# Kernel optimization log

Measured on AMD Instinct MI355X. Metric: run time of the kernel, lower is better.

## Reference

```python
import jax, jax.numpy as jnp
import numpy as np

N_NODES = 10000
N_EDGES = 640000
N_GRAPHS = 64
IN_FEAT = 128
HID = (128, 128)
NUM_CLASS = 10


def setup_inputs() -> dict:
    key = jax.random.key(0)
    ks = jax.random.split(key, 10)
    x = jax.random.normal(ks[0], (N_NODES, IN_FEAT), dtype=jnp.float32)
    edge_index = jax.random.randint(ks[1], (2, N_EDGES), 0, N_NODES, dtype=jnp.int64)
    batch = jnp.sort(jax.random.randint(ks[2], (N_NODES,), 0, N_GRAPHS, dtype=jnp.int64))
    # GCNConv weights (PyG applies x @ W then propagates, bias added after aggregation)
    s1 = 1.0 / np.sqrt(IN_FEAT)
    s2 = 1.0 / np.sqrt(HID[0])
    s3 = 1.0 / np.sqrt(HID[1])
    W1 = jax.random.uniform(ks[3], (IN_FEAT, HID[0]), jnp.float32, -s1, s1)
    b1 = jnp.zeros((HID[0],), jnp.float32)
    W2 = jax.random.uniform(ks[4], (HID[0], HID[1]), jnp.float32, -s2, s2)
    b2 = jnp.zeros((HID[1],), jnp.float32)
    Wlin = jax.random.uniform(ks[5], (HID[1], NUM_CLASS), jnp.float32, -s3, s3)
    blin = jax.random.uniform(ks[6], (NUM_CLASS,), jnp.float32, -s3, s3)
    return {"x": x, "edge_index": edge_index, "batch": batch,
            "W1": W1, "b1": b1, "W2": W2, "b2": b2, "Wlin": Wlin, "blin": blin}


def _gcn_conv(x, src, dst, W, b):
    # GCNConv with self-loops and symmetric normalization:
    # out[i] = sum_{(j->i) in E} d[j]^{-1/2} d[i]^{-1/2} (x_j W) + d[i]^{-1} (x_i W) + b
    # where d = in-degree (on dst) + 1 for the self-loop.
    h = x @ W                                                      # [N, F]
    ones = jnp.ones(src.shape[0], dtype=h.dtype)
    deg = jax.ops.segment_sum(ones, dst, num_segments=x.shape[0]) + 1.0
    dinv = jax.lax.rsqrt(deg)                                      # [N]
    norm = dinv[src] * dinv[dst]                                   # [E]
    agg = jax.ops.segment_sum(h[src] * norm[:, None], dst, num_segments=x.shape[0])
    agg = agg + h * (dinv * dinv)[:, None]                         # self-loop term
    return agg + b


def _global_mean_pool(x, batch, num_graphs):
    sums = jax.ops.segment_sum(x, batch, num_segments=num_graphs)          # [G, F]
    cnt = jax.ops.segment_sum(jnp.ones(x.shape[0], x.dtype), batch, num_segments=num_graphs)
    return sums / jnp.maximum(cnt, 1.0)[:, None]


def reference(x, edge_index, batch, W1, b1, W2, b2, Wlin, blin):
    src, dst = edge_index[0], edge_index[1]
    h = jax.nn.relu(_gcn_conv(x, src, dst, W1, b1))
    h = jax.nn.relu(_gcn_conv(h, src, dst, W2, b2))
    g = _global_mean_pool(h, batch, N_GRAPHS)      # [G, hid1]
    return g @ Wlin + blin                          # [G, num_class]
```

## Files before the change

kernel.cpp:

```cpp
#include <hip/hip_runtime.h>

#define NN 10000
#define NE 640000
#define NG 64
#define NF 128
#define NC 10
#define TMR 16
#define TKC 32
#define NB 250
#define BSZ 40
#define G1 512
#define ECHUNK 1250
#define CAP 32
#define CCAP 3072
#define NSL 64
#define MAXD 192


__device__ __forceinline__ unsigned short f2bf(float f) {
    unsigned int u = __float_as_uint(f);
    return (unsigned short)((u + 0x7FFF + ((u >> 16) & 1)) >> 16);
}
__device__ __forceinline__ float bf_lo(unsigned int p) {
    return __uint_as_float(p << 16);
}
__device__ __forceinline__ float bf_hi(unsigned int p) {
    return __uint_as_float(p & 0xFFFF0000u);
}

__device__ __forceinline__ int detect64(const int* w, long span) {
    int lane = threadIdx.x & 63;
    long e = (long)lane * (span - 1) / 63;
    return (__ballot(w[2 * e + 1] != 0) == 0ULL) ? 1 : 0;
}

__device__ __forceinline__ int ld_idx(const void* p, long i, int is64) {
    return is64 ? (int)((const long long*)p)[i] : ((const int*)p)[i];
}

__global__ __launch_bounds__(256) void k_prep(const void* __restrict__ ei,
                                              const void* __restrict__ batch,
                                              int* __restrict__ bh,
                                              int* __restrict__ ebuf,
                                              float* __restrict__ outacc,
                                              float* __restrict__ cntinv) {
    int is64 = detect64((const int*)ei, NE);
    __shared__ int hist[256];
    __shared__ int cur[256];
    int tid = threadIdx.x;
    hist[tid] = 0;
    __syncthreads();
    if (blockIdx.x < 8) {
        float* base = outacc + (size_t)blockIdx.x * 8 * NG * NC;
        for (int i = tid; i < 8 * NG * NC; i += 256) base[i] = 0.f;
    }
    if (blockIdx.x == 8 && tid < NG) {
        int isb = detect64((const int*)batch, NN / 2);
        int lo0 = 0, hi0 = NN;
        while (lo0 < hi0) {
            int m = (lo0 + hi0) >> 1;
            if (ld_idx(batch, m, isb) < tid) lo0 = m + 1; else hi0 = m;
        }
        int lo1 = lo0, hi1 = NN;
        while (lo1 < hi1) {
            int m = (lo1 + hi1) >> 1;
            if (ld_idx(batch, m, isb) < tid + 1) lo1 = m + 1; else hi1 = m;
        }
        cntinv[tid] = 1.0f / fmaxf((float)(lo1 - lo0), 1.0f);
    }
    int e0 = blockIdx.x * ECHUNK;
    int dstv[5], srcv[5];
#pragma unroll
    for (int i = 0; i < 5; ++i) {
        int r = tid + i * 256;
        if (r < ECHUNK) {
            long e = (long)e0 + r;
            dstv[i] = ld_idx(ei, (long)NE + e, is64);
            srcv[i] = ld_idx(ei, e, is64);
            atomicAdd(&hist[dstv[i] / BSZ], 1);
        } else {
            dstv[i] = -1; srcv[i] = 0;
        }
    }
    __syncthreads();
    if (tid < NB) {
        bh[tid * G1 + blockIdx.x] = min(hist[tid], CAP);
        cur[tid] = (tid * G1 + blockIdx.x) * CAP;
    }
    __syncthreads();
#pragma unroll
    for (int i = 0; i < 5; ++i) {
        if (tid + i * 256 < ECHUNK) {
            int dst = dstv[i], src = srcv[i];
            int b = dst / BSZ;
            int p = atomicAdd(&cur[b], 1);
            int lim = (b * G1 + blockIdx.x) * CAP + CAP;
            if (p < lim) ebuf[p] = ((dst - b * BSZ) << 14) | src;
        }
    }
}

__global__ __launch_bounds__(256) void k_csr(const int* __restrict__ ebuf,
                                             const int* __restrict__ bh,
                                             int* __restrict__ coff,
                                             int* __restrict__ deg,
                                             float* __restrict__ dinv,
                                             unsigned short* __restrict__ csrc) {
    __shared__ int scnt[G1];
    __shared__ int cbase[G1];
    __shared__ int wsum[4];
    __shared__ int eb[CCAP];
    __shared__ int dcount[BSZ];
    __shared__ int cur[BSZ];
    int b = blockIdx.x, tid = threadIdx.x;
    int lane = tid & 63, wv = tid >> 6;
    for (int i = tid; i < G1; i += 256) scnt[i] = bh[b * G1 + i];
    if (tid < BSZ) dcount[tid] = 0;
    __syncthreads();
    int v0 = scnt[2 * tid], v1 = scnt[2 * tid + 1];
    int lsum = v0 + v1;
    int pref = lsum;
    for (int o = 1; o < 64; o <<= 1) {
        int t = __shfl_up(pref, o, 64);
        if (lane >= o) pref += t;
    }
    if (lane == 63) wsum[wv] = pref;
    __syncthreads();
    int off = 0;
#pragma unroll
    for (int j = 0; j < 4; ++j) if (j < wv) off += wsum[j];
    int ex = pref - lsum + off;
    cbase[2 * tid] = ex;
    cbase[2 * tid + 1] = ex + v0;
    int tot = wsum[0] + wsum[1] + wsum[2] + wsum[3];
    if (tot > CCAP) tot = CCAP;
    __syncthreads();
#pragma unroll
    for (int cp = 0; cp < 2; ++cp) {
        int cell = 2 * tid + cp;
        int c = scnt[cell], lb = cbase[cell];
        int gb = (b * G1 + cell) * CAP;
        if (lb + c > CCAP) c = max(0, CCAP - lb);
        for (int i = 0; i < c; ++i) eb[lb + i] = ebuf[gb + i];
    }
    __syncthreads();
    for (int i = tid; i < tot; i += 256)
        atomicAdd(&dcount[eb[i] >> 14], 1);
    __syncthreads();
    if (tid < 64) {
        int d = (tid < BSZ) ? dcount[tid] : 0;
        int pr = d;
        for (int o = 1; o < 64; o <<= 1) {
            int t = __shfl_up(pr, o, 64);
            if (tid >= o) pr += t;
        }
        if (tid < BSZ) {
            int st = pr - d;
            cur[tid] = b * CCAP + st;
            coff[b * BSZ + tid] = b * CCAP + st;
            deg[b * BSZ + tid] = d;
            dinv[b * BSZ + tid] = rsqrtf((float)d + 1.0f);
        }
    }
    __syncthreads();
    for (int i = tid; i < tot; i += 256) {
        int pk = eb[i];
        int p = atomicAdd(&cur[pk >> 14], 1);
        csrc[p] = (unsigned short)(pk & 16383);
    }
}

__global__ __launch_bounds__(256) void k_gemm(const float* __restrict__ X,
                                              const float* __restrict__ W,
                                              const float* __restrict__ dinv,
                                              unsigned short* __restrict__ Y,
                                              int nrows) {
    __shared__ float sX[TKC * 20];
    __shared__ float sW[32 * 132];
    int tid = threadIdx.x;
    int rg = tid & 7;
    int cg = tid >> 3;
    int m0 = blockIdx.x * TMR;
    float acc[2][4] = {{0.f}};
    for (int kc = 0; kc < NF / TKC; ++kc) {
        int k0 = kc * TKC;
        if (tid < 128) {
            int row = tid >> 3, kq = tid & 7;
            int mm = m0 + row; if (mm > nrows - 1) mm = nrows - 1;
            float4 v = *(const float4*)(X + (size_t)mm * NF + k0 + kq * 4);
            sX[(kq * 4 + 0) * 20 + row] = v.x;
            sX[(kq * 4 + 1) * 20 + row] = v.y;
            sX[(kq * 4 + 2) * 20 + row] = v.z;
            sX[(kq * 4 + 3) * 20 + row] = v.w;
        }
#pragma unroll
        for (int j = 0; j < 4; ++j) {
            int idx = tid + 256 * j;
            int k = idx >> 5, cq = idx & 31;
            float4 v = *(const float4*)(W + (size_t)(k0 + k) * NF + cq * 4);
            *(float4*)(sW + cq * 132 + k * 4) = v;
        }
        __syncthreads();
#pragma unroll 8
        for (int k = 0; k < TKC; ++k) {
            float2 xf = *(const float2*)(sX + k * 20 + rg * 2);
            float4 wf = *(const float4*)(sW + cg * 132 + k * 4);
            acc[0][0] = fmaf(xf.x, wf.x, acc[0][0]);
            acc[0][1] = fmaf(xf.x, wf.y, acc[0][1]);
            acc[0][2] = fmaf(xf.x, wf.z, acc[0][2]);
            acc[0][3] = fmaf(xf.x, wf.w, acc[0][3]);
            acc[1][0] = fmaf(xf.y, wf.x, acc[1][0]);
            acc[1][1] = fmaf(xf.y, wf.y, acc[1][1]);
            acc[1][2] = fmaf(xf.y, wf.z, acc[1][2]);
            acc[1][3] = fmaf(xf.y, wf.w, acc[1][3]);
        }
        __syncthreads();
    }
#pragma unroll
    for (int r = 0; r < 2; ++r) {
        int m = m0 + rg * 2 + r;
        if (m < nrows) {
            float ds = dinv[m];
            ushort4 h;
            h.x = f2bf(acc[r][0] * ds);
            h.y = f2bf(acc[r][1] * ds);
            h.z = f2bf(acc[r][2] * ds);
            h.w = f2bf(acc[r][3] * ds);
            *(ushort4*)(Y + (size_t)m * NF + cg * 4) = h;
        }
    }
}

__device__ __forceinline__ void gacc_node(const unsigned short* __restrict__ G,
                                          const unsigned short* __restrict__ csrc,
                                          unsigned short* ls,
                                          int beg, int end, int q, int f, int lane,
                                          float a[8]) {
    int dg = end - beg;
    int nst = min(dg, MAXD);
    for (int i = lane; i < nst; i += 64) ls[i] = csrc[beg + i];
    int vi = q;
    int nfull = nst & ~31;
    for (; vi < nfull; vi += 32) {
        int s[8];
#pragma unroll
        for (int j = 0; j < 8; ++j) s[j] = ls[vi + 4 * j];
        uint4 p[8];
#pragma unroll
        for (int j = 0; j < 8; ++j)
            p[j] = ((const uint4*)(G + (size_t)s[j] * NF))[f];
#pragma unroll
        for (int j = 0; j < 8; ++j) {
            a[0] += bf_lo(p[j].x); a[1] += bf_hi(p[j].x);
            a[2] += bf_lo(p[j].y); a[3] += bf_hi(p[j].y);
            a[4] += bf_lo(p[j].z); a[5] += bf_hi(p[j].z);
            a[6] += bf_lo(p[j].w); a[7] += bf_hi(p[j].w);
        }
    }
    int nfull16 = nst & ~15;
    for (; vi < nfull16; vi += 16) {
        int s[4];
#pragma unroll
        for (int j = 0; j < 4; ++j) s[j] = ls[vi + 4 * j];
        uint4 p[4];
#pragma unroll
        for (int j = 0; j < 4; ++j)
            p[j] = ((const uint4*)(G + (size_t)s[j] * NF))[f];
#pragma unroll
        for (int j = 0; j < 4; ++j) {
            a[0] += bf_lo(p[j].x); a[1] += bf_hi(p[j].x);
            a[2] += bf_lo(p[j].y); a[3] += bf_hi(p[j].y);
            a[4] += bf_lo(p[j].z); a[5] += bf_hi(p[j].z);
            a[6] += bf_lo(p[j].w); a[7] += bf_hi(p[j].w);
        }
    }
    int npad = (nst + 3) & ~3;
    for (; vi < npad; vi += 4) {
        int s = ls[min(vi, nst - 1)];
        uint4 p = ((const uint4*)(G + (size_t)s * NF))[f];
        if (vi < nst) {
            a[0] += bf_lo(p.x); a[1] += bf_hi(p.x);
            a[2] += bf_lo(p.y); a[3] += bf_hi(p.y);
            a[4] += bf_lo(p.z); a[5] += bf_hi(p.z);
            a[6] += bf_lo(p.w); a[7] += bf_hi(p.w);
        }
    }
    for (int e2 = beg + MAXD + q; e2 < end; e2 += 4) {
        int s = csrc[e2];
        uint4 p = ((const uint4*)(G + (size_t)s * NF))[f];
        a[0] += bf_lo(p.x); a[1] += bf_hi(p.x);
        a[2] += bf_lo(p.y); a[3] += bf_hi(p.y);
        a[4] += bf_lo(p.z); a[5] += bf_hi(p.z);
        a[6] += bf_lo(p.w); a[7] += bf_hi(p.w);
    }
#pragma unroll
    for (int j = 0; j < 8; ++j) a[j] += __shfl_xor(a[j], 16);
#pragma unroll
    for (int j = 0; j < 8; ++j) a[j] += __shfl_xor(a[j], 32);
}

__global__ __launch_bounds__(256, 4) void k_gather(const unsigned short* __restrict__ G,
                                                   const int* __restrict__ off,
                                                   const int* __restrict__ dg,
                                                   const unsigned short* __restrict__ csrc,
                                                   const float* __restrict__ dinv,
                                                   const float* __restrict__ bias,
                                                   float* __restrict__ OUT) {
    __shared__ unsigned short lsbuf[4][MAXD];
    int wid = threadIdx.x >> 6, lane = threadIdx.x & 63;
    int q = lane >> 4, f = lane & 15;
    int n = blockIdx.x * 4 + wid;
    if (n >= NN) return;
    int beg = off[n], end = beg + dg[n];
    float din = dinv[n];
    float a[8] = {0.f, 0.f, 0.f, 0.f, 0.f, 0.f, 0.f, 0.f};
    gacc_node(G, csrc, lsbuf[wid], beg, end, q, f, lane, a);
    if (q == 0) {
        uint4 sp = ((const uint4*)(G + (size_t)n * NF))[f];
        float4 b0 = ((const float4*)bias)[2 * f];
        float4 b1 = ((const float4*)bias)[2 * f + 1];
        float4 o0, o1;
        o0.x = fmaxf(fmaf(din, a[0] + bf_lo(sp.x), b0.x), 0.f);
        o0.y = fmaxf(fmaf(din, a[1] + bf_hi(sp.x), b0.y), 0.f);
        o0.z = fmaxf(fmaf(din, a[2] + bf_lo(sp.y), b0.z), 0.f);
        o0.w = fmaxf(fmaf(din, a[3] + bf_hi(sp.y), b0.w), 0.f);
        o1.x = fmaxf(fmaf(din, a[4] + bf_lo(sp.z), b1.x), 0.f);
        o1.y = fmaxf(fmaf(din, a[5] + bf_hi(sp.z), b1.y), 0.f);
        o1.z = fmaxf(fmaf(din, a[6] + bf_lo(sp.w), b1.z), 0.f);
        o1.w = fmaxf(fmaf(din, a[7] + bf_hi(sp.w), b1.w), 0.f);
        ((float4*)(OUT + (size_t)n * NF))[2 * f] = o0;
        ((float4*)(OUT + (size_t)n * NF))[2 * f + 1] = o1;
    }
}

__global__ __launch_bounds__(256, 4) void k_gatherpool(const unsigned short* __restrict__ G,
                                                       const int* __restrict__ off,
                                                       const int* __restrict__ dg,
                                                       const unsigned short* __restrict__ csrc,
                                                       const float* __restrict__ dinv,
                                                       const float* __restrict__ bias,
                                                       const void* __restrict__ batch,
                                                       const float* __restrict__ Wl,
                                                       const float* __restrict__ cntinv,
                                                       float* __restrict__ outacc) {
    __shared__ float sWl2[8 * NC * 16];
    __shared__ unsigned short lsbuf[4][MAXD];
    int tid = threadIdx.x;
    for (int i = tid; i < 8 * NC * 16; i += 256) {
        int j = i / (NC * 16);
        int r = i - j * (NC * 16);
        int c = r >> 4, f0 = r & 15;
        sWl2[i] = Wl[(f0 * 8 + j) * NC + c];
    }
    int isb64 = detect64((const int*)batch, NN / 2);
    int wid = tid >> 6, lane = tid & 63;
    int q = lane >> 4, f = lane & 15;
    int n = blockIdx.x * 4 + wid;
    int beg = off[n], end = beg + dg[n];
    float din = dinv[n];
    float a[8] = {0.f, 0.f, 0.f, 0.f, 0.f, 0.f, 0.f, 0.f};
    __syncthreads();
    gacc_node(G, csrc, lsbuf[wid], beg, end, q, f, lane, a);
    int g = ld_idx(batch, n, isb64);
    uint4 sp = ((const uint4*)(G + (size_t)n * NF))[f];
    float4 b0 = ((const float4*)bias)[2 * f];
    float4 b1 = ((const float4*)bias)[2 * f + 1];
    float h[8];
    h[0] = fmaxf(fmaf(din, a[0] + bf_lo(sp.x), b0.x), 0.f);
    h[1] = fmaxf(fmaf(din, a[1] + bf_hi(sp.x), b0.y), 0.f);
    h[2] = fmaxf(fmaf(din, a[2] + bf_lo(sp.y), b0.z), 0.f);
    h[3] = fmaxf(fmaf(din, a[3] + bf_hi(sp.y), b0.w), 0.f);
    h[4] = fmaxf(fmaf(din, a[4] + bf_lo(sp.z), b1.x), 0.f);
    h[5] = fmaxf(fmaf(din, a[5] + bf_hi(sp.z), b1.y), 0.f);
    h[6] = fmaxf(fmaf(din, a[6] + bf_lo(sp.w), b1.z), 0.f);
    h[7] = fmaxf(fmaf(din, a[7] + bf_hi(sp.w), b1.w), 0.f);
    float p[NC];
#pragma unroll
    for (int c = 0; c < NC; ++c) p[c] = 0.f;
#pragma unroll
    for (int j = 0; j < 8; ++j) {
        const float* wrow = sWl2 + j * (NC * 16) + f;
#pragma unroll
        for (int c = 0; c < NC; ++c) p[c] = fmaf(h[j], wrow[c * 16], p[c]);
    }
#pragma unroll
    for (int c = 0; c < NC; ++c) {
        p[c] += __shfl_xor(p[c], 1);
        p[c] += __shfl_xor(p[c], 2);
        p[c] += __shfl_xor(p[c], 4);
        p[c] += __shfl_xor(p[c], 8);
    }
    if (lane == 0) {
        float ci = cntinv[g];
        float* dst = outacc + (size_t)(blockIdx.x & (NSL - 1)) * NG * NC + g * NC;
#pragma unroll
        for (int c = 0; c < NC; ++c) atomicAdd(dst + c, p[c] * ci);
    }
}

__global__ __launch_bounds__(256) void k_fin(const float* __restrict__ outacc,
                                             const float* __restrict__ bl,
                                             float* __restrict__ out) {
    int tid = threadIdx.x;
    for (int i = tid; i < NG * NC; i += 256) {
        float s = 0.f;
#pragma unroll 8
        for (int sl = 0; sl < NSL; ++sl) s += outacc[(size_t)sl * NG * NC + i];
        out[i] = s + bl[i % NC];
    }
}

extern "C" void kernel_launch(void* const* d_in, const int* in_sizes, int n_in,
                              void* d_out, int out_size, void* d_ws, size_t ws_size,
                              hipStream_t stream) {
    const float* x  = (const float*)d_in[0];
    const void*  ei = d_in[1];
    const void*  bt = d_in[2];
    const float* W1 = (const float*)d_in[3];
    const float* b1 = (const float*)d_in[4];
    const float* W2 = (const float*)d_in[5];
    const float* b2 = (const float*)d_in[6];
    const float* Wl = (const float*)d_in[7];
    const float* bl = (const float*)d_in[8];

    char* ws = (char*)d_ws;
    int*            coff   = (int*)(ws + 0);
    int*            deg    = (int*)(ws + 40000);
    float*          dinv   = (float*)(ws + 80000);
    float*          outacc = (float*)(ws + 120000);
    float*          cntinv = (float*)(ws + 283840);
    unsigned short* csrc   = (unsigned short*)(ws + 284160);
    unsigned short* Gb     = (unsigned short*)(ws + 2201088);
    float*          bufB   = (float*)(ws + 4761088);
    int*            bh     = (int*)(ws + 2201088);
    int*            ebuf   = (int*)(ws + 4761088);

    k_prep<<<G1, 256, 0, stream>>>(ei, bt, bh, ebuf, outacc, cntinv);
    k_csr <<<NB, 256, 0, stream>>>(ebuf, bh, coff, deg, dinv, csrc);

    k_gemm<<<(NN + TMR - 1) / TMR, 256, 0, stream>>>(x, W1, dinv, Gb, NN);
    k_gather<<<(NN + 3) / 4, 256, 0, stream>>>(Gb, coff, deg, csrc, dinv, b1, bufB);
    k_gemm<<<(NN + TMR - 1) / TMR, 256, 0, stream>>>(bufB, W2, dinv, Gb, NN);
    k_gatherpool<<<(NN + 3) / 4, 256, 0, stream>>>(Gb, coff, deg, csrc, dinv, b2,
                                                   bt, Wl, cntinv, outacc);
    k_fin<<<1, 256, 0, stream>>>(outacc, bl, (float*)d_out);
}
```

Before: 165.9 us.

## Fuse first-layer GEMM into prep kernel and move source scaling into gather

The first-layer X@W1 GEMM now runs as extra blocks of the edge-preprocessing kernel, so it no longer waits for the degree computation. The source-side dinv scaling is therefore applied per edge in the first gather, using dinv values staged in shared memory alongside the neighbour indices. This drops one kernel launch and its serialization, at the cost of an extra per-edge dinv lookup and FMA in the first gather. Workspace offsets are rearranged so the GEMM output no longer overlaps buffers the prep kernel is still writing.

```diff
diff --git a/kernel.cpp b/kernel.cpp
--- a/kernel.cpp
+++ b/kernel.cpp
@@ -10,6 +10,7 @@
 #define NB 250
 #define BSZ 40
 #define G1 512
+#define GEMMB ((NN + TMR - 1) / TMR)
 #define ECHUNK 1250
 #define CAP 32
 #define CCAP 3072
@@ -38,21 +39,80 @@
     return is64 ? (int)((const long long*)p)[i] : ((const int*)p)[i];
 }
 
-__global__ __launch_bounds__(256) void k_prep(const void* __restrict__ ei,
-                                              const void* __restrict__ batch,
-                                              int* __restrict__ bh,
-                                              int* __restrict__ ebuf,
-                                              float* __restrict__ outacc,
-                                              float* __restrict__ cntinv) {
-    int is64 = detect64((const int*)ei, NE);
+__global__ __launch_bounds__(256) void k_prepgemm(const void* __restrict__ ei,
+                                                  const void* __restrict__ batch,
+                                                  int* __restrict__ bh,
+                                                  int* __restrict__ ebuf,
+                                                  float* __restrict__ outacc,
+                                                  float* __restrict__ cntinv,
+                                                  const float* __restrict__ X,
+                                                  const float* __restrict__ W,
+                                                  unsigned short* __restrict__ Y) {
     __shared__ int hist[256];
     __shared__ int cur[256];
+    __shared__ float sX[TKC * 20];
+    __shared__ float sW[32 * 132];
     int tid = threadIdx.x;
+
+    if (blockIdx.x >= G1) {
+        int m0 = (int)(blockIdx.x - G1) * TMR;
+        int rg = tid & 7;
+        int cg = tid >> 3;
+        float acc[2][4] = {{0.f}};
+        for (int kc = 0; kc < NF / TKC; ++kc) {
+            int k0 = kc * TKC;
+            if (tid < 128) {
+                int row = tid >> 3, kq = tid & 7;
+                int mm = m0 + row; if (mm > NN - 1) mm = NN - 1;
+                float4 v = *(const float4*)(X + (size_t)mm * NF + k0 + kq * 4);
+                sX[(kq * 4 + 0) * 20 + row] = v.x;
+                sX[(kq * 4 + 1) * 20 + row] = v.y;
+                sX[(kq * 4 + 2) * 20 + row] = v.z;
+                sX[(kq * 4 + 3) * 20 + row] = v.w;
+            }
+#pragma unroll
+            for (int j = 0; j < 4; ++j) {
+                int idx = tid + 256 * j;
+                int k = idx >> 5, cq = idx & 31;
+                float4 v = *(const float4*)(W + (size_t)(k0 + k) * NF + cq * 4);
+                *(float4*)(sW + cq * 132 + k * 4) = v;
+            }
+            __syncthreads();
+#pragma unroll 8
+            for (int k = 0; k < TKC; ++k) {
+                float2 xf = *(const float2*)(sX + k * 20 + rg * 2);
+                float4 wf = *(const float4*)(sW + cg * 132 + k * 4);
+                acc[0][0] = fmaf(xf.x, wf.x, acc[0][0]);
+                acc[0][1] = fmaf(xf.x, wf.y, acc[0][1]);
+                acc[0][2] = fmaf(xf.x, wf.z, acc[0][2]);
+                acc[0][3] = fmaf(xf.x, wf.w, acc[0][3]);
+                acc[1][0] = fmaf(xf.y, wf.x, acc[1][0]);
+                acc[1][1] = fmaf(xf.y, wf.y, acc[1][1]);
+                acc[1][2] = fmaf(xf.y, wf.z, acc[1][2]);
+                acc[1][3] = fmaf(xf.y, wf.w, acc[1][3]);
+            }
+            __syncthreads();
+        }
+#pragma unroll
+        for (int r = 0; r < 2; ++r) {
+            int m = m0 + rg * 2 + r;
+            if (m < NN) {
+                ushort4 h;
+                h.x = f2bf(acc[r][0]);
+                h.y = f2bf(acc[r][1]);
+                h.z = f2bf(acc[r][2]);
+                h.w = f2bf(acc[r][3]);
+                *(ushort4*)(Y + (size_t)m * NF + cg * 4) = h;
+            }
+        }
+        return;
+    }
+
+    int is64 = detect64((const int*)ei, NE);
     hist[tid] = 0;
     __syncthreads();
-    if (blockIdx.x < 8) {
-        float* base = outacc + (size_t)blockIdx.x * 8 * NG * NC;
-        for (int i = tid; i < 8 * NG * NC; i += 256) base[i] = 0.f;
+    if (blockIdx.x == 0) {
+        for (int i = tid; i < NSL * NG * NC; i += 256) outacc[i] = 0.f;
     }
     if (blockIdx.x == 8 && tid < NG) {
         int isb = detect64((const int*)batch, NN / 2);
@@ -231,67 +291,110 @@
     }
 }
 
+template <int EDGE_SCALE>
 __device__ __forceinline__ void gacc_node(const unsigned short* __restrict__ G,
                                           const unsigned short* __restrict__ csrc,
-                                          unsigned short* ls,
+                                          const float* __restrict__ dv,
+                                          unsigned short* ls, float* lsd,
                                           int beg, int end, int q, int f, int lane,
                                           float a[8]) {
     int dg = end - beg;
     int nst = min(dg, MAXD);
-    for (int i = lane; i < nst; i += 64) ls[i] = csrc[beg + i];
+    for (int i = lane; i < nst; i += 64) {
+        unsigned short s = csrc[beg + i];
+        ls[i] = s;
+        if (EDGE_SCALE) lsd[i] = dv[s];
+    }
     int vi = q;
     int nfull = nst & ~31;
     for (; vi < nfull; vi += 32) {
-        int s[8];
-#pragma unroll
-        for (int j = 0; j < 8; ++j) s[j] = ls[vi + 4 * j];
+        int s[8]; float d[8];
+#pragma unroll
+        for (int j = 0; j < 8; ++j) {
+            s[j] = ls[vi + 4 * j];
+            d[j] = EDGE_SCALE ? lsd[vi + 4 * j] : 1.f;
+        }
         uint4 p[8];
 #pragma unroll
         for (int j = 0; j < 8; ++j)
             p[j] = ((const uint4*)(G + (size_t)s[j] * NF))[f];
 #pragma unroll
         for (int j = 0; j < 8; ++j) {
-            a[0] += bf_lo(p[j].x); a[1] += bf_hi(p[j].x);
-            a[2] += bf_lo(p[j].y); a[3] += bf_hi(p[j].y);
-            a[4] += bf_lo(p[j].z); a[5] += bf_hi(p[j].z);
-            a[6] += bf_lo(p[j].w); a[7] += bf_hi(p[j].w);
+            if (EDGE_SCALE) {
+                a[0] = fmaf(d[j], bf_lo(p[j].x), a[0]); a[1] = fmaf(d[j], bf_hi(p[j].x), a[1]);
+                a[2] = fmaf(d[j], bf_lo(p[j].y), a[2]); a[3] = fmaf(d[j], bf_hi(p[j].y), a[3]);
+                a[4] = fmaf(d[j], bf_lo(p[j].z), a[4]); a[5] = fmaf(d[j], bf_hi(p[j].z), a[5]);
+                a[6] = fmaf(d[j], bf_lo(p[j].w), a[6]); a[7] = fmaf(d[j], bf_hi(p[j].w), a[7]);
+            } else {
+                a[0] += bf_lo(p[j].x); a[1] += bf_hi(p[j].x);
+                a[2] += bf_lo(p[j].y); a[3] += bf_hi(p[j].y);
+                a[4] += bf_lo(p[j].z); a[5] += bf_hi(p[j].z);
+                a[6] += bf_lo(p[j].w); a[7] += bf_hi(p[j].w);
+            }
         }
     }
     int nfull16 = nst & ~15;
     for (; vi < nfull16; vi += 16) {
-        int s[4];
-#pragma unroll
-        for (int j = 0; j < 4; ++j) s[j] = ls[vi + 4 * j];
+        int s[4]; float d[4];
+#pragma unroll
+        for (int j = 0; j < 4; ++j) {
+            s[j] = ls[vi + 4 * j];
+            d[j] = EDGE_SCALE ? lsd[vi + 4 * j] : 1.f;
+        }
         uint4 p[4];
 #pragma unroll
         for (int j = 0; j < 4; ++j)
             p[j] = ((const uint4*)(G + (size_t)s[j] * NF))[f];
 #pragma unroll
         for (int j = 0; j < 4; ++j) {
-            a[0] += bf_lo(p[j].x); a[1] += bf_hi(p[j].x);
-            a[2] += bf_lo(p[j].y); a[3] += bf_hi(p[j].y);
-            a[4] += bf_lo(p[j].z); a[5] += bf_hi(p[j].z);
-            a[6] += bf_lo(p[j].w); a[7] += bf_hi(p[j].w);
+            if (EDGE_SCALE) {
+                a[0] = fmaf(d[j], bf_lo(p[j].x), a[0]); a[1] = fmaf(d[j], bf_hi(p[j].x), a[1]);
+                a[2] = fmaf(d[j], bf_lo(p[j].y), a[2]); a[3] = fmaf(d[j], bf_hi(p[j].y), a[3]);
+                a[4] = fmaf(d[j], bf_lo(p[j].z), a[4]); a[5] = fmaf(d[j], bf_hi(p[j].z), a[5]);
+                a[6] = fmaf(d[j], bf_lo(p[j].w), a[6]); a[7] = fmaf(d[j], bf_hi(p[j].w), a[7]);
+            } else {
+                a[0] += bf_lo(p[j].x); a[1] += bf_hi(p[j].x);
+                a[2] += bf_lo(p[j].y); a[3] += bf_hi(p[j].y);
+                a[4] += bf_lo(p[j].z); a[5] += bf_hi(p[j].z);
+                a[6] += bf_lo(p[j].w); a[7] += bf_hi(p[j].w);
+            }
         }
     }
     int npad = (nst + 3) & ~3;
     for (; vi < npad; vi += 4) {
-        int s = ls[min(vi, nst - 1)];
+        int ii = min(vi, nst - 1);
+        int s = ls[ii];
+        float d = EDGE_SCALE ? lsd[ii] : 1.f;
         uint4 p = ((const uint4*)(G + (size_t)s * NF))[f];
         if (vi < nst) {
+            if (EDGE_SCALE) {
+                a[0] = fmaf(d, bf_lo(p.x), a[0]); a[1] = fmaf(d, bf_hi(p.x), a[1]);
+                a[2] = fmaf(d, bf_lo(p.y), a[2]); a[3] = fmaf(d, bf_hi(p.y), a[3]);
+                a[4] = fmaf(d, bf_lo(p.z), a[4]); a[5] = fmaf(d, bf_hi(p.z), a[5]);
+                a[6] = fmaf(d, bf_lo(p.w), a[6]); a[7] = fmaf(d, bf_hi(p.w), a[7]);
+            } else {
+                a[0] += bf_lo(p.x); a[1] += bf_hi(p.x);
+                a[2] += bf_lo(p.y); a[3] += bf_hi(p.y);
+                a[4] += bf_lo(p.z); a[5] += bf_hi(p.z);
+                a[6] += bf_lo(p.w); a[7] += bf_hi(p.w);
+            }
+        }
+    }
+    for (int e2 = beg + MAXD + q; e2 < end; e2 += 4) {
+        int s = csrc[e2];
+        float d = EDGE_SCALE ? dv[s] : 1.f;
+        uint4 p = ((const uint4*)(G + (size_t)s * NF))[f];
+        if (EDGE_SCALE) {
+            a[0] = fmaf(d, bf_lo(p.x), a[0]); a[1] = fmaf(d, bf_hi(p.x), a[1]);
+            a[2] = fmaf(d, bf_lo(p.y), a[2]); a[3] = fmaf(d, bf_hi(p.y), a[3]);
+            a[4] = fmaf(d, bf_lo(p.z), a[4]); a[5] = fmaf(d, bf_hi(p.z), a[5]);
+            a[6] = fmaf(d, bf_lo(p.w), a[6]); a[7] = fmaf(d, bf_hi(p.w), a[7]);
+        } else {
             a[0] += bf_lo(p.x); a[1] += bf_hi(p.x);
             a[2] += bf_lo(p.y); a[3] += bf_hi(p.y);
             a[4] += bf_lo(p.z); a[5] += bf_hi(p.z);
             a[6] += bf_lo(p.w); a[7] += bf_hi(p.w);
         }
-    }
-    for (int e2 = beg + MAXD + q; e2 < end; e2 += 4) {
-        int s = csrc[e2];
-        uint4 p = ((const uint4*)(G + (size_t)s * NF))[f];
-        a[0] += bf_lo(p.x); a[1] += bf_hi(p.x);
-        a[2] += bf_lo(p.y); a[3] += bf_hi(p.y);
-        a[4] += bf_lo(p.z); a[5] += bf_hi(p.z);
-        a[6] += bf_lo(p.w); a[7] += bf_hi(p.w);
     }
 #pragma unroll
     for (int j = 0; j < 8; ++j) a[j] += __shfl_xor(a[j], 16);
@@ -307,6 +410,7 @@
                                                    const float* __restrict__ bias,
                                                    float* __restrict__ OUT) {
     __shared__ unsigned short lsbuf[4][MAXD];
+    __shared__ float lsdbuf[4][MAXD];
     int wid = threadIdx.x >> 6, lane = threadIdx.x & 63;
     int q = lane >> 4, f = lane & 15;
     int n = blockIdx.x * 4 + wid;
@@ -314,20 +418,20 @@
     int beg = off[n], end = beg + dg[n];
     float din = dinv[n];
     float a[8] = {0.f, 0.f, 0.f, 0.f, 0.f, 0.f, 0.f, 0.f};
-    gacc_node(G, csrc, lsbuf[wid], beg, end, q, f, lane, a);
+    gacc_node<1>(G, csrc, dinv, lsbuf[wid], lsdbuf[wid], beg, end, q, f, lane, a);
     if (q == 0) {
         uint4 sp = ((const uint4*)(G + (size_t)n * NF))[f];
         float4 b0 = ((const float4*)bias)[2 * f];
         float4 b1 = ((const float4*)bias)[2 * f + 1];
         float4 o0, o1;
-        o0.x = fmaxf(fmaf(din, a[0] + bf_lo(sp.x), b0.x), 0.f);
-        o0.y = fmaxf(fmaf(din, a[1] + bf_hi(sp.x), b0.y), 0.f);
-        o0.z = fmaxf(fmaf(din, a[2] + bf_lo(sp.y), b0.z), 0.f);
-        o0.w = fmaxf(fmaf(din, a[3] + bf_hi(sp.y), b0.w), 0.f);
-        o1.x = fmaxf(fmaf(din, a[4] + bf_lo(sp.z), b1.x), 0.f);
-        o1.y = fmaxf(fmaf(din, a[5] + bf_hi(sp.z), b1.y), 0.f);
-        o1.z = fmaxf(fmaf(din, a[6] + bf_lo(sp.w), b1.z), 0.f);
-        o1.w = fmaxf(fmaf(din, a[7] + bf_hi(sp.w), b1.w), 0.f);
+        o0.x = fmaxf(fmaf(din, fmaf(din, bf_lo(sp.x), a[0]), b0.x), 0.f);
+        o0.y = fmaxf(fmaf(din, fmaf(din, bf_hi(sp.x), a[1]), b0.y), 0.f);
+        o0.z = fmaxf(fmaf(din, fmaf(din, bf_lo(sp.y), a[2]), b0.z), 0.f);
+        o0.w = fmaxf(fmaf(din, fmaf(din, bf_hi(sp.y), a[3]), b0.w), 0.f);
+        o1.x = fmaxf(fmaf(din, fmaf(din, bf_lo(sp.z), a[4]), b1.x), 0.f);
+        o1.y = fmaxf(fmaf(din, fmaf(din, bf_hi(sp.z), a[5]), b1.y), 0.f);
+        o1.z = fmaxf(fmaf(din, fmaf(din, bf_lo(sp.w), a[6]), b1.z), 0.f);
+        o1.w = fmaxf(fmaf(din, fmaf(din, bf_hi(sp.w), a[7]), b1.w), 0.f);
         ((float4*)(OUT + (size_t)n * NF))[2 * f] = o0;
         ((float4*)(OUT + (size_t)n * NF))[2 * f + 1] = o1;
     }
@@ -360,7 +464,7 @@
     float din = dinv[n];
     float a[8] = {0.f, 0.f, 0.f, 0.f, 0.f, 0.f, 0.f, 0.f};
     __syncthreads();
-    gacc_node(G, csrc, lsbuf[wid], beg, end, q, f, lane, a);
+    gacc_node<0>(G, csrc, dinv, lsbuf[wid], (float*)nullptr, beg, end, q, f, lane, a);
     int g = ld_idx(batch, n, isb64);
     uint4 sp = ((const uint4*)(G + (size_t)n * NF))[f];
     float4 b0 = ((const float4*)bias)[2 * f];
@@ -430,17 +534,17 @@
     float*          outacc = (float*)(ws + 120000);
     float*          cntinv = (float*)(ws + 283840);
     unsigned short* csrc   = (unsigned short*)(ws + 284160);
-    unsigned short* Gb     = (unsigned short*)(ws + 2201088);
-    float*          bufB   = (float*)(ws + 4761088);
-    int*            bh     = (int*)(ws + 2201088);
-    int*            ebuf   = (int*)(ws + 4761088);
-
-    k_prep<<<G1, 256, 0, stream>>>(ei, bt, bh, ebuf, outacc, cntinv);
+    int*            bh     = (int*)(ws + 1820160);
+    unsigned short* Gb     = (unsigned short*)(ws + 2344448);
+    int*            ebuf   = (int*)(ws + 4904448);
+    float*          bufB   = (float*)(ws + 4904448);
+
+    k_prepgemm<<<G1 + GEMMB, 256, 0, stream>>>(ei, bt, bh, ebuf, outacc, cntinv,
+                                               x, W1, Gb);
     k_csr <<<NB, 256, 0, stream>>>(ebuf, bh, coff, deg, dinv, csrc);
 
-    k_gemm<<<(NN + TMR - 1) / TMR, 256, 0, stream>>>(x, W1, dinv, Gb, NN);
     k_gather<<<(NN + 3) / 4, 256, 0, stream>>>(Gb, coff, deg, csrc, dinv, b1, bufB);
-    k_gemm<<<(NN + TMR - 1) / TMR, 256, 0, stream>>>(bufB, W2, dinv, Gb, NN);
+    k_gemm<<<GEMMB, 256, 0, stream>>>(bufB, W2, dinv, Gb, NN);
     k_gatherpool<<<(NN + 3) / 4, 256, 0, stream>>>(Gb, coff, deg, csrc, dinv, b2,
                                                    bt, Wl, cntinv, outacc);
     k_fin<<<1, 256, 0, stream>>>(outacc, bl, (float*)d_out);
```

After: 159.7 us, median of 3. 3.8% less time.
